# Optimization experiments

Hardware: AMD Instinct MI355X
Metric: run time of the kernel (lower is better)

Reference implementation:

```python
import jax, jax.numpy as jnp
import numpy as np

N = 50000      # nodes
E = 800000     # edges (before self-loops)
F_IN = 256     # num_features
H = 4          # heads
C = 64         # hidden_channels
HC = H * C     # 256
L = 2          # n_layers
G = 128        # num graphs
DENSE = 64     # dense_nhid
NCLS = 2       # num_classes
NEG_SLOPE = 0.2
BN_EPS = 1e-5


def setup_inputs() -> dict:
    key = jax.random.key(0)
    ks = jax.random.split(key, 16)
    s = 0.1
    inp = {}
    inp['x'] = jax.random.normal(ks[0], (N, F_IN), jnp.float32)
    inp['edge_index'] = jax.random.randint(ks[1], (2, E), 0, N, dtype=jnp.int32)
    inp['batch'] = jnp.sort(jax.random.randint(ks[2], (N,), 0, G, dtype=jnp.int32))
    # conv1 (GATConv: lin weight [in, H*C], att vectors [H, C], bias [H*C])
    inp['W1'] = jax.random.normal(ks[3], (F_IN, HC), jnp.float32) * s
    inp['as1'] = jax.random.normal(ks[4], (H, C), jnp.float32) * s
    inp['ad1'] = jax.random.normal(ks[5], (H, C), jnp.float32) * s
    inp['b1'] = jnp.zeros((HC,), jnp.float32)
    # stacked params for the L inner conv layers + their BatchNorms
    inp['Wl'] = jax.random.normal(ks[6], (L, HC, HC), jnp.float32) * s
    inp['asl'] = jax.random.normal(ks[7], (L, H, C), jnp.float32) * s
    inp['adl'] = jax.random.normal(ks[8], (L, H, C), jnp.float32) * s
    inp['bl'] = jnp.zeros((L, HC), jnp.float32)
    inp['bng'] = jnp.ones((L, HC), jnp.float32)
    inp['bnb'] = jnp.zeros((L, HC), jnp.float32)
    # bn1 + MLP head
    inp['bn1g'] = jnp.ones((HC,), jnp.float32)
    inp['bn1b'] = jnp.zeros((HC,), jnp.float32)
    inp['lin1W'] = jax.random.normal(ks[9], (HC, DENSE), jnp.float32) * s
    inp['lin1b'] = jnp.zeros((DENSE,), jnp.float32)
    inp['lin2W'] = jax.random.normal(ks[10], (DENSE, DENSE), jnp.float32) * s
    inp['lin2b'] = jnp.zeros((DENSE,), jnp.float32)
    inp['lin3W'] = jax.random.normal(ks[11], (DENSE, NCLS), jnp.float32) * s
    inp['lin3b'] = jnp.zeros((NCLS,), jnp.float32)
    return inp


def _gat(x, src, dst, W, a_src, a_dst, b):
    # GATConv: h_j = W x_j; e_ij = LeakyReLU(a_src.h_j + a_dst.h_i);
    # alpha = softmax over incoming edges of node i; out_i = sum_j alpha*h_j (concat heads) + bias
    h = (x @ W).reshape(-1, H, C)                       # [N, H, C]
    es = jnp.sum(h * a_src, axis=-1)                    # [N, H]
    ed = jnp.sum(h * a_dst, axis=-1)                    # [N, H]
    e = jax.nn.leaky_relu(es[src] + ed[dst], NEG_SLOPE) # [E2, H]
    m = jax.ops.segment_max(e, dst, num_segments=N)
    ex = jnp.exp(e - m[dst])
    ssum = jax.ops.segment_sum(ex, dst, num_segments=N)
    alpha = ex / (ssum[dst] + 1e-16)                    # [E2, H]
    agg = jax.ops.segment_sum(h[src] * alpha[:, :, None], dst, num_segments=N)
    return agg.reshape(-1, HC) + b


def _bn(x, g, b):
    # BatchNorm1d in training mode (biased batch variance)
    mu = jnp.mean(x, axis=0)
    var = jnp.mean((x - mu) ** 2, axis=0)
    return (x - mu) / jnp.sqrt(var + BN_EPS) * g + b


def reference(x, edge_index, batch, W1, as1, ad1, b1, Wl, asl, adl, bl, bng, bnb,
              bn1g, bn1b, lin1W, lin1b, lin2W, lin2b, lin3W, lin3b):
    loops = jnp.arange(N, dtype=edge_index.dtype)
    src = jnp.concatenate([edge_index[0], loops])  # GATConv adds self-loops
    dst = jnp.concatenate([edge_index[1], loops])
    h = jax.nn.relu(_gat(x, src, dst, W1, as1, ad1, b1))
    for i in range(L):
        h = jax.nn.relu(_bn(_gat(h, src, dst, Wl[i], asl[i], adl[i], bl[i]), bng[i], bnb[i]))
    cnt = jax.ops.segment_sum(jnp.ones((N,), h.dtype), batch, num_segments=G)
    pooled = jax.ops.segment_sum(h, batch, num_segments=G) / jnp.maximum(cnt, 1.0)[:, None]
    z = _bn(pooled, bn1g, bn1b)  # dropout is identity in eval
    z = jax.nn.relu(z @ lin1W + lin1b)
    z = jax.nn.relu(z @ lin2W + lin2b)
    z = jax.nn.relu(z @ lin3W + lin3b)
    out = jax.nn.softmax(z, axis=1)
    return (out, pooled)
```

## Files before the change

kernel.cpp:

```cpp
#include <hip/hip_runtime.h>

#define N_NODES 50000
#define E_EDGES 800000
#define E2 (E_EDGES + N_NODES)
#define HC 256
#define NHEAD 4
#define GG 128
#define DENSE 64
#define NCLS 2
#define BN_EPS 1e-5f
#define NEG_SLOPE 0.2f
#define NEG_BIG -1e30f

typedef __attribute__((ext_vector_type(8))) short bf16x8;
typedef __attribute__((ext_vector_type(4))) float f32x4;

__device__ __forceinline__ unsigned short f2bf(float f) {
    unsigned int u = __float_as_uint(f);
    u = (u + 0x7FFFu + ((u >> 16) & 1u)) >> 16;
    return (unsigned short)u;
}
__device__ __forceinline__ float bf2f(unsigned short h) {
    return __uint_as_float(((unsigned int)h) << 16);
}
__device__ __forceinline__ float lrelu(float e) {
    return (e >= 0.f) ? e : NEG_SLOPE * e;
}
__device__ __forceinline__ void accum8(float acc[8], uint4 v, float w) {
    acc[0] = fmaf(w, __uint_as_float(v.x << 16), acc[0]);
    acc[1] = fmaf(w, __uint_as_float(v.x & 0xffff0000u), acc[1]);
    acc[2] = fmaf(w, __uint_as_float(v.y << 16), acc[2]);
    acc[3] = fmaf(w, __uint_as_float(v.y & 0xffff0000u), acc[3]);
    acc[4] = fmaf(w, __uint_as_float(v.z << 16), acc[4]);
    acc[5] = fmaf(w, __uint_as_float(v.z & 0xffff0000u), acc[5]);
    acc[6] = fmaf(w, __uint_as_float(v.w << 16), acc[6]);
    acc[7] = fmaf(w, __uint_as_float(v.w & 0xffff0000u), acc[7]);
}

__global__ __launch_bounds__(64) void pack_b_kernel(const float* __restrict__ W1,
                                                    const float* __restrict__ Wl,
                                                    unsigned short* __restrict__ Bpk) {
    int l = threadIdx.x;
    int mat = blockIdx.x >> 7;
    int g = blockIdx.x & 127;
    const float* W = (mat == 0) ? W1 : Wl + (size_t)(mat - 1) * HC * HC;
    int ks = g >> 4, ct = g & 15;
    int col = ct * 16 + (l & 15);
    int k0 = ks * 32 + (l >> 4) * 8;
    unsigned short v[8];
#pragma unroll
    for (int j = 0; j < 8; ++j) v[j] = f2bf(W[(size_t)(k0 + j) * HC + col]);
    ushort4* q = reinterpret_cast<ushort4*>(Bpk + ((size_t)mat * 128 * 512) + ((size_t)g * 64 + l) * 8);
    q[0] = make_ushort4(v[0], v[1], v[2], v[3]);
    q[1] = make_ushort4(v[4], v[5], v[6], v[7]);
}

#define GBM 128
__global__ __launch_bounds__(256) void gemm_mfma_kernel(const unsigned short* __restrict__ A,
                                                        const float* __restrict__ A32,
                                                        const unsigned short* __restrict__ Bpk,
                                                        const float* __restrict__ prm,
                                                        unsigned short* __restrict__ C, int M) {
    __shared__ unsigned short As[GBM * 256];
    int tid = threadIdx.x;
    int lane = tid & 63, wid = tid >> 6;
    int row0 = blockIdx.x * GBM;
#pragma unroll
    for (int i = 0; i < 16; ++i) {
        int idx = tid + i * 256;
        int row = idx >> 5, c16 = idx & 31;
        int grow = row0 + row;
        uint4 v = make_uint4(0u, 0u, 0u, 0u);
        if (A32) {
            if (grow < M) {
                const float4* p = reinterpret_cast<const float4*>(A32 + (size_t)grow * HC + c16 * 8);
                float4 a = p[0], b = p[1];
                v.x = (unsigned int)f2bf(a.x) | ((unsigned int)f2bf(a.y) << 16);
                v.y = (unsigned int)f2bf(a.z) | ((unsigned int)f2bf(a.w) << 16);
                v.z = (unsigned int)f2bf(b.x) | ((unsigned int)f2bf(b.y) << 16);
                v.w = (unsigned int)f2bf(b.z) | ((unsigned int)f2bf(b.w) << 16);
            }
        } else {
            if (grow < M) v = *reinterpret_cast<const uint4*>(A + (size_t)grow * HC + c16 * 8);
            if (prm) {
                int ch = c16 * 8;
                const float4 s0 = *reinterpret_cast<const float4*>(prm + ch);
                const float4 s1 = *reinterpret_cast<const float4*>(prm + ch + 4);
                const float4 t0 = *reinterpret_cast<const float4*>(prm + HC + ch);
                const float4 t1 = *reinterpret_cast<const float4*>(prm + HC + ch + 4);
                float f0 = fmaxf(fmaf(__uint_as_float(v.x << 16),          s0.x, t0.x), 0.f);
                float f1 = fmaxf(fmaf(__uint_as_float(v.x & 0xffff0000u),  s0.y, t0.y), 0.f);
                float f2 = fmaxf(fmaf(__uint_as_float(v.y << 16),          s0.z, t0.z), 0.f);
                float f3 = fmaxf(fmaf(__uint_as_float(v.y & 0xffff0000u),  s0.w, t0.w), 0.f);
                float f4 = fmaxf(fmaf(__uint_as_float(v.z << 16),          s1.x, t1.x), 0.f);
                float f5 = fmaxf(fmaf(__uint_as_float(v.z & 0xffff0000u),  s1.y, t1.y), 0.f);
                float f6 = fmaxf(fmaf(__uint_as_float(v.w << 16),          s1.z, t1.z), 0.f);
                float f7 = fmaxf(fmaf(__uint_as_float(v.w & 0xffff0000u),  s1.w, t1.w), 0.f);
                v.x = (unsigned int)f2bf(f0) | ((unsigned int)f2bf(f1) << 16);
                v.y = (unsigned int)f2bf(f2) | ((unsigned int)f2bf(f3) << 16);
                v.z = (unsigned int)f2bf(f4) | ((unsigned int)f2bf(f5) << 16);
                v.w = (unsigned int)f2bf(f6) | ((unsigned int)f2bf(f7) << 16);
            }
        }
        int byteoff = row * 512 + c16 * 16;
        byteoff ^= (row & 7) << 4;
        *reinterpret_cast<uint4*>((char*)As + byteoff) = v;
    }
    __syncthreads();

    f32x4 acc[8][4];
#pragma unroll
    for (int rt = 0; rt < 8; ++rt)
#pragma unroll
        for (int c = 0; c < 4; ++c) acc[rt][c] = (f32x4){0.f, 0.f, 0.f, 0.f};

    int arow = lane & 15;
    int asub = (lane >> 4) * 16;
#pragma unroll
    for (int ks = 0; ks < 8; ++ks) {
        const unsigned short* bp = Bpk + ((size_t)(ks * 16 + wid * 4) * 512 + lane * 8);
        bf16x8 b0 = *reinterpret_cast<const bf16x8*>(bp);
        bf16x8 b1 = *reinterpret_cast<const bf16x8*>(bp + 512);
        bf16x8 b2 = *reinterpret_cast<const bf16x8*>(bp + 1024);
        bf16x8 b3 = *reinterpret_cast<const bf16x8*>(bp + 1536);
#pragma unroll
        for (int rt = 0; rt < 8; ++rt) {
            int mrow = rt * 16 + arow;
            int abyte = mrow * 512 + ks * 64 + asub;
            abyte ^= (mrow & 7) << 4;
            bf16x8 a = *reinterpret_cast<const bf16x8*>((char*)As + abyte);
            acc[rt][0] = __builtin_amdgcn_mfma_f32_16x16x32_bf16(a, b0, acc[rt][0], 0, 0, 0);
            acc[rt][1] = __builtin_amdgcn_mfma_f32_16x16x32_bf16(a, b1, acc[rt][1], 0, 0, 0);
            acc[rt][2] = __builtin_amdgcn_mfma_f32_16x16x32_bf16(a, b2, acc[rt][2], 0, 0, 0);
            acc[rt][3] = __builtin_amdgcn_mfma_f32_16x16x32_bf16(a, b3, acc[rt][3], 0, 0, 0);
        }
    }
    int ccol = lane & 15;
#pragma unroll
    for (int rt = 0; rt < 8; ++rt) {
        int crow0 = row0 + rt * 16 + (lane >> 4) * 4;
#pragma unroll
        for (int c = 0; c < 4; ++c) {
            int gcol = (wid * 4 + c) * 16 + ccol;
#pragma unroll
            for (int r = 0; r < 4; ++r) {
                int grow = crow0 + r;
                if (grow < M) C[(size_t)grow * HC + gcol] = f2bf(acc[rt][c][r]);
            }
        }
    }
}

__global__ __launch_bounds__(256) void esed_kernel(const unsigned short* __restrict__ h,
                                                   const float* __restrict__ avs,
                                                   const float* __restrict__ avd,
                                                   float* __restrict__ es, float* __restrict__ ed) {
    int tid = threadIdx.x;
    int lane = tid & 63, wid = tid >> 6;
    int node = blockIdx.x * 4 + wid;
    if (node >= N_NODES) return;
    int ch0 = lane * 4;
    ushort4 hv = *reinterpret_cast<const ushort4*>(h + (size_t)node * HC + ch0);
    float4 sa = *reinterpret_cast<const float4*>(avs + ch0);
    float4 da = *reinterpret_cast<const float4*>(avd + ch0);
    float h0 = bf2f(hv.x), h1 = bf2f(hv.y), h2 = bf2f(hv.z), h3 = bf2f(hv.w);
    float vs = h0 * sa.x + h1 * sa.y + h2 * sa.z + h3 * sa.w;
    float vd = h0 * da.x + h1 * da.y + h2 * da.z + h3 * da.w;
#pragma unroll
    for (int m = 1; m < 16; m <<= 1) {
        vs += __shfl_xor(vs, m, 64);
        vd += __shfl_xor(vd, m, 64);
    }
    if ((lane & 15) == 0) {
        es[node * NHEAD + (lane >> 4)] = vs;
        ed[node * NHEAD + (lane >> 4)] = vd;
    }
}

__global__ void init_deg_kernel(int* __restrict__ deg) {
    int i = blockIdx.x * blockDim.x + threadIdx.x;
    if (i < N_NODES) deg[i] = 1;
}
__global__ void count_edges_kernel(const int* __restrict__ dst, int* __restrict__ deg) {
    int i = blockIdx.x * blockDim.x + threadIdx.x;
    if (i < E_EDGES) atomicAdd(&deg[dst[i]], 1);
}
__global__ __launch_bounds__(1024) void scan1_kernel(const int* __restrict__ deg,
                                                     int* __restrict__ rs, int* __restrict__ bsum) {
    __shared__ int wsum[16];
    int t = threadIdx.x, lane = t & 63, wid = t >> 6;
    int i = blockIdx.x * 1024 + t;
    int v = (i < N_NODES) ? deg[i] : 0;
    int x = v;
#pragma unroll
    for (int off = 1; off < 64; off <<= 1) {
        int y = __shfl_up(x, off, 64);
        if (lane >= off) x += y;
    }
    if (lane == 63) wsum[wid] = x;
    __syncthreads();
    if (wid == 0) {
        int s = (lane < 16) ? wsum[lane] : 0;
#pragma unroll
        for (int off = 1; off < 16; off <<= 1) {
            int y = __shfl_up(s, off, 64);
            if (lane >= off) s += y;
        }
        if (lane < 16) wsum[lane] = s;
    }
    __syncthreads();
    int woff = wid ? wsum[wid - 1] : 0;
    if (i <= N_NODES) rs[i] = woff + x - v;
    if (t == 1023) bsum[blockIdx.x] = wsum[15];
}
__global__ void scan2_kernel(int* __restrict__ bsum, int nb) {
    int l = threadIdx.x;
    int v = (l < nb) ? bsum[l] : 0;
    int x = v;
#pragma unroll
    for (int off = 1; off < 64; off <<= 1) {
        int y = __shfl_up(x, off, 64);
        if (l >= off) x += y;
    }
    if (l < nb) bsum[l] = x - v;
}
__global__ void scan3_kernel(int* __restrict__ rs, const int* __restrict__ bsum,
                             int* __restrict__ cursor, int* __restrict__ csr) {
    int i = blockIdx.x * blockDim.x + threadIdx.x;
    if (i <= N_NODES) {
        int v = rs[i] + bsum[i >> 10];
        rs[i] = v;
        if (i < N_NODES) {
            csr[v] = i;
            cursor[i] = v + 1;
        }
    }
}
__global__ void scatter_edges_kernel(const int* __restrict__ src, const int* __restrict__ dst,
                                     int* __restrict__ cursor, int* __restrict__ csr) {
    int i = blockIdx.x * blockDim.x + threadIdx.x;
    if (i < E_EDGES) {
        int pos = atomicAdd(&cursor[dst[i]], 1);
        csr[pos] = src[i];
    }
}

__global__ __launch_bounds__(256) void smprep_kernel(const float* __restrict__ es,
                                                     const float* __restrict__ ed,
                                                     const int* __restrict__ rs,
                                                     const int* __restrict__ csr,
                                                     float* __restrict__ alpha) {
    int tid = threadIdx.x;
    int lane = tid & 63, wid = tid >> 6;
    int node = blockIdx.x * 4 + wid;
    if (node >= N_NODES) return;
    int head = lane >> 4, slot = lane & 15;
    float edn = ed[node * NHEAD + head];
    int beg = rs[node], end = rs[node + 1];
    float m = NEG_BIG, s = 0.f;
    for (int i = beg + slot; i < end; i += 16) {
        float e = lrelu(es[csr[i] * NHEAD + head] + edn);
        alpha[(size_t)i * NHEAD + head] = e;
        float mn = fmaxf(m, e);
        s = s * __expf(m - mn) + __expf(e - mn);
        m = mn;
    }
#pragma unroll
    for (int off = 1; off < 16; off <<= 1) {
        float mo = __shfl_xor(m, off, 64);
        float so = __shfl_xor(s, off, 64);
        float mn = fmaxf(m, mo);
        s = s * __expf(m - mn) + so * __expf(mo - mn);
        m = mn;
    }
    float inv = 1.f / (s + 1e-16f);
    for (int i = beg + slot; i < end; i += 16) {
        float e = alpha[(size_t)i * NHEAD + head];
        alpha[(size_t)i * NHEAD + head] = __expf(e - m) * inv;
    }
}

__global__ __launch_bounds__(256) void gat_agg_kernel(const unsigned short* __restrict__ hlin,
                                                      const float* __restrict__ alpha,
                                                      const int* __restrict__ rs,
                                                      const int* __restrict__ csr,
                                                      const float* __restrict__ bias,
                                                      unsigned short* __restrict__ out, int do_relu) {
    int tid = threadIdx.x;
    int lane = tid & 63, wid = tid >> 6;
    int node = blockIdx.x * 8 + wid * 2 + (lane >> 5);
    int hl = lane & 31;
    int ch0 = hl * 8;
    int head = hl >> 3;
    bool valid = node < N_NODES;
    int beg = valid ? rs[node] : 0;
    int end = valid ? rs[node + 1] : 0;
    float acc[8] = {};
    int idx = beg;
    for (; idx + 4 <= end; idx += 4) {
        int s0 = csr[idx], s1 = csr[idx + 1], s2 = csr[idx + 2], s3 = csr[idx + 3];
        float p0 = alpha[(size_t)idx * NHEAD + head];
        float p1 = alpha[(size_t)(idx + 1) * NHEAD + head];
        float p2 = alpha[(size_t)(idx + 2) * NHEAD + head];
        float p3 = alpha[(size_t)(idx + 3) * NHEAD + head];
        uint4 v0 = *reinterpret_cast<const uint4*>(hlin + (size_t)s0 * HC + ch0);
        uint4 v1 = *reinterpret_cast<const uint4*>(hlin + (size_t)s1 * HC + ch0);
        uint4 v2 = *reinterpret_cast<const uint4*>(hlin + (size_t)s2 * HC + ch0);
        uint4 v3 = *reinterpret_cast<const uint4*>(hlin + (size_t)s3 * HC + ch0);
        accum8(acc, v0, p0);
        accum8(acc, v1, p1);
        accum8(acc, v2, p2);
        accum8(acc, v3, p3);
    }
    for (; idx < end; ++idx) {
        int s0 = csr[idx];
        float p0 = alpha[(size_t)idx * NHEAD + head];
        uint4 v0 = *reinterpret_cast<const uint4*>(hlin + (size_t)s0 * HC + ch0);
        accum8(acc, v0, p0);
    }
    if (!valid) return;
    const float4 bva = *reinterpret_cast<const float4*>(bias + ch0);
    const float4 bvb = *reinterpret_cast<const float4*>(bias + ch0 + 4);
    float o[8];
    o[0] = acc[0] + bva.x; o[1] = acc[1] + bva.y; o[2] = acc[2] + bva.z; o[3] = acc[3] + bva.w;
    o[4] = acc[4] + bvb.x; o[5] = acc[5] + bvb.y; o[6] = acc[6] + bvb.z; o[7] = acc[7] + bvb.w;
    if (do_relu) {
#pragma unroll
        for (int j = 0; j < 8; ++j) o[j] = fmaxf(o[j], 0.f);
    }
    uint4 w;
    w.x = (unsigned int)f2bf(o[0]) | ((unsigned int)f2bf(o[1]) << 16);
    w.y = (unsigned int)f2bf(o[2]) | ((unsigned int)f2bf(o[3]) << 16);
    w.z = (unsigned int)f2bf(o[4]) | ((unsigned int)f2bf(o[5]) << 16);
    w.w = (unsigned int)f2bf(o[6]) | ((unsigned int)f2bf(o[7]) << 16);
    *reinterpret_cast<uint4*>(out + (size_t)node * HC + ch0) = w;
}

#define BN_RPB 49
__global__ __launch_bounds__(256) void bn_stats_kernel(const unsigned short* __restrict__ x,
                                                       float* __restrict__ sums) {
    __shared__ float lds[8][512];
    int tid = threadIdx.x;
    int c = tid & 31;
    int rt = tid >> 5;
    int r0 = blockIdx.x * BN_RPB;
    int r1 = min(N_NODES, r0 + BN_RPB);
    int ch = c * 8;
    float s[8] = {}, s2[8] = {};
    for (int r = r0 + rt; r < r1; r += 8) {
        const ushort4* p = reinterpret_cast<const ushort4*>(x + (size_t)r * HC + ch);
        ushort4 va = p[0], vb = p[1];
        unsigned short in[8] = {va.x, va.y, va.z, va.w, vb.x, vb.y, vb.z, vb.w};
#pragma unroll
        for (int j = 0; j < 8; ++j) {
            float v = bf2f(in[j]);
            s[j] += v; s2[j] += v * v;
        }
    }
#pragma unroll
    for (int j = 0; j < 8; ++j) {
        lds[rt][ch + j] = s[j];
        lds[rt][256 + ch + j] = s2[j];
    }
    __syncthreads();
#pragma unroll
    for (int e = tid; e < 512; e += 256) {
        float v = 0.f;
#pragma unroll
        for (int r = 0; r < 8; ++r) v += lds[r][e];
        atomicAdd(&sums[e], v);
    }
}
__global__ void bn_finalize_kernel(const float* __restrict__ sums, const float* __restrict__ g,
                                   const float* __restrict__ b, float* __restrict__ prm) {
    int t = threadIdx.x;
    float mean = sums[t] / (float)N_NODES;
    float var = sums[HC + t] / (float)N_NODES - mean * mean;
    var = fmaxf(var, 0.f);
    float scale = g[t] * rsqrtf(var + BN_EPS);
    prm[t] = scale;
    prm[HC + t] = b[t] - mean * scale;
}

#define POOL_RPB 32
__global__ __launch_bounds__(256) void pool_kernel(const unsigned short* __restrict__ h,
                                                   const float* __restrict__ prm,
                                                   const int* __restrict__ batch,
                                                   float* __restrict__ psum) {
    int tid = threadIdx.x;
    int ct = tid & 63;
    int rt = tid >> 6;
    int r0 = blockIdx.x * POOL_RPB;
    int r1 = min(N_NODES, r0 + POOL_RPB);
    int ch = ct * 4;
    const float4 sc = *reinterpret_cast<const float4*>(prm + ch);
    const float4 sh = *reinterpret_cast<const float4*>(prm + HC + ch);
    float a0 = 0.f, a1 = 0.f, a2 = 0.f, a3 = 0.f;
    int gcur = -1;
    for (int r = r0 + rt; r < r1; r += 4) {
        int g = batch[r];
        if (g != gcur) {
            if (gcur >= 0) {
                atomicAdd(&psum[gcur * HC + ch + 0], a0);
                atomicAdd(&psum[gcur * HC + ch + 1], a1);
                atomicAdd(&psum[gcur * HC + ch + 2], a2);
                atomicAdd(&psum[gcur * HC + ch + 3], a3);
            }
            a0 = a1 = a2 = a3 = 0.f; gcur = g;
        }
        ushort4 hv = *reinterpret_cast<const ushort4*>(h + (size_t)r * HC + ch);
        a0 += fmaxf(fmaf(bf2f(hv.x), sc.x, sh.x), 0.f);
        a1 += fmaxf(fmaf(bf2f(hv.y), sc.y, sh.y), 0.f);
        a2 += fmaxf(fmaf(bf2f(hv.z), sc.z, sh.z), 0.f);
        a3 += fmaxf(fmaf(bf2f(hv.w), sc.w, sh.w), 0.f);
    }
    if (gcur >= 0) {
        atomicAdd(&psum[gcur * HC + ch + 0], a0);
        atomicAdd(&psum[gcur * HC + ch + 1], a1);
        atomicAdd(&psum[gcur * HC + ch + 2], a2);
        atomicAdd(&psum[gcur * HC + ch + 3], a3);
    }
}
__global__ void pool_fin_kernel(const float* __restrict__ psum, const int* __restrict__ batch,
                                float* __restrict__ pooled) {
    int g = blockIdx.x, t = threadIdx.x;
    int lo = 0, hi = N_NODES;
    while (lo < hi) { int mid = (lo + hi) >> 1; if (batch[mid] <= g) lo = mid + 1; else hi = mid; }
    int lo2 = 0, hi2 = N_NODES;
    while (lo2 < hi2) { int mid = (lo2 + hi2) >> 1; if (batch[mid] <= g - 1) lo2 = mid + 1; else hi2 = mid; }
    float cf = fmaxf((float)(lo - lo2), 1.f);
    pooled[g * HC + t] = psum[g * HC + t] / cf;
}

__global__ __launch_bounds__(256) void head_kernel(const float* __restrict__ pooled,
                                                   const float* __restrict__ bn1g,
                                                   const float* __restrict__ bn1b,
                                                   const float* __restrict__ l1W,
                                                   const float* __restrict__ l1b,
                                                   const float* __restrict__ l2W,
                                                   const float* __restrict__ l2b,
                                                   const float* __restrict__ l3W,
                                                   const float* __restrict__ l3b,
                                                   float* __restrict__ out) {
    __shared__ float z0[HC];
    __shared__ float z1[DENSE];
    __shared__ float z2[DENSE];
    int r = blockIdx.x;
    int t = threadIdx.x;
    float s = 0.f, s2 = 0.f;
    for (int rr = 0; rr < GG; ++rr) {
        float v = pooled[rr * HC + t];
        s += v; s2 += v * v;
    }
    float mean = s / (float)GG;
    float var = fmaxf(s2 / (float)GG - mean * mean, 0.f);
    float scale = bn1g[t] * rsqrtf(var + BN_EPS);
    float shift = bn1b[t] - mean * scale;
    z0[t] = pooled[r * HC + t] * scale + shift;
    __syncthreads();
    if (t < DENSE) {
        float a = l1b[t];
        for (int k = 0; k < HC; ++k) a += z0[k] * l1W[k * DENSE + t];
        z1[t] = fmaxf(a, 0.f);
    }
    __syncthreads();
    if (t < DENSE) {
        float a = l2b[t];
        for (int k = 0; k < DENSE; ++k) a += z1[k] * l2W[k * DENSE + t];
        z2[t] = fmaxf(a, 0.f);
    }
    __syncthreads();
    if (t == 0) {
        float o0 = l3b[0], o1 = l3b[1];
        for (int k = 0; k < DENSE; ++k) {
            o0 += z2[k] * l3W[k * NCLS + 0];
            o1 += z2[k] * l3W[k * NCLS + 1];
        }
        o0 = fmaxf(o0, 0.f); o1 = fmaxf(o1, 0.f);
        float mx = fmaxf(o0, o1);
        float e0 = __expf(o0 - mx), e1 = __expf(o1 - mx);
        float inv = 1.f / (e0 + e1);
        out[r * NCLS + 0] = e0 * inv;
        out[r * NCLS + 1] = e1 * inv;
    }
}

extern "C" void kernel_launch(void* const* d_in, const int* in_sizes, int n_in,
                              void* d_out, int out_size, void* d_ws, size_t ws_size,
                              hipStream_t stream) {
    const float* x     = (const float*)d_in[0];
    const int*   ei    = (const int*)d_in[1];
    const int*   srcp  = ei;
    const int*   dstp  = ei + E_EDGES;
    const int*   batch = (const int*)d_in[2];
    const float* W1    = (const float*)d_in[3];
    const float* as1   = (const float*)d_in[4];
    const float* ad1   = (const float*)d_in[5];
    const float* b1    = (const float*)d_in[6];
    const float* Wl    = (const float*)d_in[7];
    const float* asl   = (const float*)d_in[8];
    const float* adl   = (const float*)d_in[9];
    const float* bl    = (const float*)d_in[10];
    const float* bng   = (const float*)d_in[11];
    const float* bnb   = (const float*)d_in[12];
    const float* bn1g  = (const float*)d_in[13];
    const float* bn1b  = (const float*)d_in[14];
    const float* l1W   = (const float*)d_in[15];
    const float* l1b   = (const float*)d_in[16];
    const float* l2W   = (const float*)d_in[17];
    const float* l2b   = (const float*)d_in[18];
    const float* l3W   = (const float*)d_in[19];
    const float* l3b   = (const float*)d_in[20];

    float* outp   = (float*)d_out;
    float* pooled = outp + GG * NCLS;

    char* w = (char*)d_ws;
    auto alloc = [&](size_t bytes) -> void* {
        void* p = (void*)w;
        w += (bytes + 255) & ~(size_t)255;
        return p;
    };
    unsigned short* h0  = (unsigned short*)alloc(sizeof(short) * (size_t)N_NODES * HC);
    unsigned short* h1  = (unsigned short*)alloc(sizeof(short) * (size_t)N_NODES * HC);
    unsigned short* h2  = (unsigned short*)alloc(sizeof(short) * (size_t)N_NODES * HC);
    unsigned short* Bpk = (unsigned short*)alloc(sizeof(short) * 3 * 128 * 64 * 8);
    float* es     = (float*)alloc(sizeof(float) * (size_t)N_NODES * NHEAD);
    float* ed     = (float*)alloc(sizeof(float) * (size_t)N_NODES * NHEAD);
    float* alpha  = (float*)alloc(sizeof(float) * (size_t)E2 * NHEAD);
    int*   rs     = (int*)alloc(sizeof(int) * (N_NODES + 1));
    int*   deg    = (int*)alloc(sizeof(int) * N_NODES);
    int*   csr    = (int*)alloc(sizeof(int) * E2);
    int*   bsum   = (int*)alloc(sizeof(int) * 64);
    float* bnsums = (float*)alloc(sizeof(float) * 2 * HC);
    float* bnprm  = (float*)alloc(sizeof(float) * 2 * HC);
    float* psum   = (float*)alloc(sizeof(float) * GG * HC);

    const int nblk_nodes = (N_NODES + 255) / 256;
    const int nblk_edges = (E_EDGES + 255) / 256;
    const int nblk_wave4 = (N_NODES + 3) / 4;
    const int nblk_wave8 = (N_NODES + 7) / 8;
    const int nscan = (N_NODES + 1023) / 1024;
    const int nblk_bn   = (N_NODES + BN_RPB - 1) / BN_RPB;
    const int nblk_pool = (N_NODES + POOL_RPB - 1) / POOL_RPB;

    pack_b_kernel<<<384, 64, 0, stream>>>(W1, Wl, Bpk);

    init_deg_kernel<<<nblk_nodes, 256, 0, stream>>>(deg);
    count_edges_kernel<<<nblk_edges, 256, 0, stream>>>(dstp, deg);
    scan1_kernel<<<nscan, 1024, 0, stream>>>(deg, rs, bsum);
    scan2_kernel<<<1, 64, 0, stream>>>(bsum, nscan);
    scan3_kernel<<<(N_NODES + 256) / 256, 256, 0, stream>>>(rs, bsum, deg, csr);
    scatter_edges_kernel<<<nblk_edges, 256, 0, stream>>>(srcp, dstp, deg, csr);

    const int ggrid = (N_NODES + GBM - 1) / GBM;

    gemm_mfma_kernel<<<ggrid, 256, 0, stream>>>(nullptr, x, Bpk, nullptr, h1, N_NODES);
    esed_kernel<<<nblk_wave4, 256, 0, stream>>>(h1, as1, ad1, es, ed);
    smprep_kernel<<<nblk_wave4, 256, 0, stream>>>(es, ed, rs, csr, alpha);
    gat_agg_kernel<<<nblk_wave8, 256, 0, stream>>>(h1, alpha, rs, csr, b1, h0, 1);

    gemm_mfma_kernel<<<ggrid, 256, 0, stream>>>(h0, nullptr, Bpk + 128 * 512, nullptr, h1, N_NODES);
    esed_kernel<<<nblk_wave4, 256, 0, stream>>>(h1, asl, adl, es, ed);
    smprep_kernel<<<nblk_wave4, 256, 0, stream>>>(es, ed, rs, csr, alpha);
    gat_agg_kernel<<<nblk_wave8, 256, 0, stream>>>(h1, alpha, rs, csr, bl, h2, 0);
    hipMemsetAsync(bnsums, 0, sizeof(float) * 2 * HC, stream);
    bn_stats_kernel<<<nblk_bn, 256, 0, stream>>>(h2, bnsums);
    bn_finalize_kernel<<<1, 256, 0, stream>>>(bnsums, bng, bnb, bnprm);

    gemm_mfma_kernel<<<ggrid, 256, 0, stream>>>(h2, nullptr, Bpk + 2 * 128 * 512, bnprm, h1, N_NODES);
    esed_kernel<<<nblk_wave4, 256, 0, stream>>>(h1, asl + HC, adl + HC, es, ed);
    smprep_kernel<<<nblk_wave4, 256, 0, stream>>>(es, ed, rs, csr, alpha);
    gat_agg_kernel<<<nblk_wave8, 256, 0, stream>>>(h1, alpha, rs, csr, bl + HC, h2, 0);
    hipMemsetAsync(bnsums, 0, sizeof(float) * 2 * HC, stream);
    bn_stats_kernel<<<nblk_bn, 256, 0, stream>>>(h2, bnsums);
    bn_finalize_kernel<<<1, 256, 0, stream>>>(bnsums, bng + HC, bnb + HC, bnprm);

    hipMemsetAsync(psum, 0, sizeof(float) * GG * HC, stream);
    pool_kernel<<<nblk_pool, 256, 0, stream>>>(h2, bnprm, batch, psum);
    pool_fin_kernel<<<GG, HC, 0, stream>>>(psum, batch, pooled);

    head_kernel<<<GG, 256, 0, stream>>>(pooled, bn1g, bn1b, l1W, l1b, l2W, l2b, l3W, l3b, outp);
}
```

Measured before the change: 543.2 us.

## Trim small kernel launches and cache edge logits in softmax prep

Several small kernels are removed. init_deg becomes a memset with the +1 self-loop folded into scan1. scan2 is folded into scan3, where each thread serially sums the preceding block sums. pool_fin is merged into head_kernel, where every block recomputes the per-graph counts by binary search. smprep now keeps the first four edge logits per lane in registers and recomputes any others, instead of writing raw logits to alpha and reading them back. The aim is less launch overhead and less global round-trip traffic, at the cost of redundant per-block work in the head and scan kernels.

```diff
diff --git a/kernel.cpp b/kernel.cpp
--- a/kernel.cpp
+++ b/kernel.cpp
@@ -177,10 +177,6 @@
     }
 }
 
-__global__ void init_deg_kernel(int* __restrict__ deg) {
-    int i = blockIdx.x * blockDim.x + threadIdx.x;
-    if (i < N_NODES) deg[i] = 1;
-}
 __global__ void count_edges_kernel(const int* __restrict__ dst, int* __restrict__ deg) {
     int i = blockIdx.x * blockDim.x + threadIdx.x;
     if (i < E_EDGES) atomicAdd(&deg[dst[i]], 1);
@@ -190,7 +186,7 @@
     __shared__ int wsum[16];
     int t = threadIdx.x, lane = t & 63, wid = t >> 6;
     int i = blockIdx.x * 1024 + t;
-    int v = (i < N_NODES) ? deg[i] : 0;
+    int v = (i < N_NODES) ? deg[i] + 1 : 0;
     int x = v;
 #pragma unroll
     for (int off = 1; off < 64; off <<= 1) {
@@ -212,23 +208,15 @@
     int woff = wid ? wsum[wid - 1] : 0;
     if (i <= N_NODES) rs[i] = woff + x - v;
     if (t == 1023) bsum[blockIdx.x] = wsum[15];
-}
-__global__ void scan2_kernel(int* __restrict__ bsum, int nb) {
-    int l = threadIdx.x;
-    int v = (l < nb) ? bsum[l] : 0;
-    int x = v;
-#pragma unroll
-    for (int off = 1; off < 64; off <<= 1) {
-        int y = __shfl_up(x, off, 64);
-        if (l >= off) x += y;
-    }
-    if (l < nb) bsum[l] = x - v;
 }
 __global__ void scan3_kernel(int* __restrict__ rs, const int* __restrict__ bsum,
                              int* __restrict__ cursor, int* __restrict__ csr) {
     int i = blockIdx.x * blockDim.x + threadIdx.x;
     if (i <= N_NODES) {
-        int v = rs[i] + bsum[i >> 10];
+        int c = i >> 10;
+        int off = 0;
+        for (int k = 0; k < c; ++k) off += bsum[k];
+        int v = rs[i] + off;
         rs[i] = v;
         if (i < N_NODES) {
             csr[v] = i;
@@ -258,9 +246,13 @@
     float edn = ed[node * NHEAD + head];
     int beg = rs[node], end = rs[node + 1];
     float m = NEG_BIG, s = 0.f;
+    float e0c = 0.f, e1c = 0.f, e2c = 0.f, e3c = 0.f;
+    int cnt = 0;
     for (int i = beg + slot; i < end; i += 16) {
         float e = lrelu(es[csr[i] * NHEAD + head] + edn);
-        alpha[(size_t)i * NHEAD + head] = e;
+        if (cnt == 0) e0c = e; else if (cnt == 1) e1c = e;
+        else if (cnt == 2) e2c = e; else if (cnt == 3) e3c = e;
+        ++cnt;
         float mn = fmaxf(m, e);
         s = s * __expf(m - mn) + __expf(e - mn);
         m = mn;
@@ -274,8 +266,12 @@
         m = mn;
     }
     float inv = 1.f / (s + 1e-16f);
-    for (int i = beg + slot; i < end; i += 16) {
-        float e = alpha[(size_t)i * NHEAD + head];
+    int k = 0;
+    for (int i = beg + slot; i < end; i += 16, ++k) {
+        float e;
+        if (k == 0) e = e0c; else if (k == 1) e = e1c;
+        else if (k == 2) e = e2c; else if (k == 3) e = e3c;
+        else e = lrelu(es[csr[i] * NHEAD + head] + edn);
         alpha[(size_t)i * NHEAD + head] = __expf(e - m) * inv;
     }
 }
@@ -421,18 +417,9 @@
         atomicAdd(&psum[gcur * HC + ch + 3], a3);
     }
 }
-__global__ void pool_fin_kernel(const float* __restrict__ psum, const int* __restrict__ batch,
-                                float* __restrict__ pooled) {
-    int g = blockIdx.x, t = threadIdx.x;
-    int lo = 0, hi = N_NODES;
-    while (lo < hi) { int mid = (lo + hi) >> 1; if (batch[mid] <= g) lo = mid + 1; else hi = mid; }
-    int lo2 = 0, hi2 = N_NODES;
-    while (lo2 < hi2) { int mid = (lo2 + hi2) >> 1; if (batch[mid] <= g - 1) lo2 = mid + 1; else hi2 = mid; }
-    float cf = fmaxf((float)(lo - lo2), 1.f);
-    pooled[g * HC + t] = psum[g * HC + t] / cf;
-}
-
-__global__ __launch_bounds__(256) void head_kernel(const float* __restrict__ pooled,
+
+__global__ __launch_bounds__(256) void head_kernel(const float* __restrict__ psum,
+                                                   const int* __restrict__ batch,
                                                    const float* __restrict__ bn1g,
                                                    const float* __restrict__ bn1b,
                                                    const float* __restrict__ l1W,
@@ -441,22 +428,35 @@
                                                    const float* __restrict__ l2b,
                                                    const float* __restrict__ l3W,
                                                    const float* __restrict__ l3b,
+                                                   float* __restrict__ pooled,
                                                    float* __restrict__ out) {
+    __shared__ float invc[GG];
     __shared__ float z0[HC];
     __shared__ float z1[DENSE];
     __shared__ float z2[DENSE];
     int r = blockIdx.x;
     int t = threadIdx.x;
+    if (t < GG) {
+        int g = t;
+        int lo = 0, hi = N_NODES;
+        while (lo < hi) { int mid = (lo + hi) >> 1; if (batch[mid] <= g) lo = mid + 1; else hi = mid; }
+        int lo2 = 0, hi2 = N_NODES;
+        while (lo2 < hi2) { int mid = (lo2 + hi2) >> 1; if (batch[mid] <= g - 1) lo2 = mid + 1; else hi2 = mid; }
+        invc[t] = 1.f / fmaxf((float)(lo - lo2), 1.f);
+    }
+    __syncthreads();
     float s = 0.f, s2 = 0.f;
     for (int rr = 0; rr < GG; ++rr) {
-        float v = pooled[rr * HC + t];
+        float v = psum[rr * HC + t] * invc[rr];
         s += v; s2 += v * v;
     }
+    float pr = psum[r * HC + t] * invc[r];
+    pooled[r * HC + t] = pr;
     float mean = s / (float)GG;
     float var = fmaxf(s2 / (float)GG - mean * mean, 0.f);
     float scale = bn1g[t] * rsqrtf(var + BN_EPS);
     float shift = bn1b[t] - mean * scale;
-    z0[t] = pooled[r * HC + t] * scale + shift;
+    z0[t] = pr * scale + shift;
     __syncthreads();
     if (t < DENSE) {
         float a = l1b[t];
@@ -536,7 +536,6 @@
     float* bnprm  = (float*)alloc(sizeof(float) * 2 * HC);
     float* psum   = (float*)alloc(sizeof(float) * GG * HC);
 
-    const int nblk_nodes = (N_NODES + 255) / 256;
     const int nblk_edges = (E_EDGES + 255) / 256;
     const int nblk_wave4 = (N_NODES + 3) / 4;
     const int nblk_wave8 = (N_NODES + 7) / 8;
@@ -546,10 +545,9 @@
 
     pack_b_kernel<<<384, 64, 0, stream>>>(W1, Wl, Bpk);
 
-    init_deg_kernel<<<nblk_nodes, 256, 0, stream>>>(deg);
+    hipMemsetAsync(deg, 0, sizeof(int) * N_NODES, stream);
     count_edges_kernel<<<nblk_edges, 256, 0, stream>>>(dstp, deg);
     scan1_kernel<<<nscan, 1024, 0, stream>>>(deg, rs, bsum);
-    scan2_kernel<<<1, 64, 0, stream>>>(bsum, nscan);
     scan3_kernel<<<(N_NODES + 256) / 256, 256, 0, stream>>>(rs, bsum, deg, csr);
     scatter_edges_kernel<<<nblk_edges, 256, 0, stream>>>(srcp, dstp, deg, csr);
 
@@ -578,7 +576,7 @@
 
     hipMemsetAsync(psum, 0, sizeof(float) * GG * HC, stream);
     pool_kernel<<<nblk_pool, 256, 0, stream>>>(h2, bnprm, batch, psum);
-    pool_fin_kernel<<<GG, HC, 0, stream>>>(psum, batch, pooled);
-
-    head_kernel<<<GG, 256, 0, stream>>>(pooled, bn1g, bn1b, l1W, l1b, l2W, l2b, l3W, l3b, outp);
-}
+
+    head_kernel<<<GG, 256, 0, stream>>>(psum, batch, bn1g, bn1b, l1W, l1b, l2W, l2b,
+                                        l3W, l3b, pooled, outp);
+}
```

Result: no change. 540.6 us (-0.5%).
